# Kernel tuning notes

Measured on AMD Instinct MI355X. Metric: run time of the kernel, lower is better.

Reference implementation:

```python
import jax, jax.numpy as jnp
import numpy as np

EPS = 1e-5
D = 32          # token embedding dim
HEADS = 8
DH = D // HEADS  # 4


def _layernorm(x, g, b):
    mu = jnp.mean(x, axis=-1, keepdims=True)
    var = jnp.mean(jnp.square(x - mu), axis=-1, keepdims=True)
    return (x - mu) / jnp.sqrt(var + EPS) * g + b


def _mhsa(x, Wqvk, W0):
    # x: [..., t, 32]; Wqvk: [96, 32]; W0: [32, 32]
    qkv = x @ Wqvk.T                                   # [..., t, 96]
    qkv = qkv.reshape(qkv.shape[:-1] + (DH, 3, HEADS))  # (d k h) layout of original rearrange
    q, k, v = qkv[..., 0, :], qkv[..., 1, :], qkv[..., 2, :]  # [..., t, d, h]
    scores = jnp.einsum('...tdh,...sdh->...hts', q, k) * (DH ** -0.5)
    attn = jax.nn.softmax(scores, axis=-1)
    out = jnp.einsum('...hts,...sdh->...thd', attn, v)  # [..., t, h, d]
    out = out.reshape(out.shape[:-2] + (D,))            # (h d) concat order
    return out @ W0.T


def setup_inputs() -> dict:
    key = jax.random.key(0)
    ks = jax.random.split(key, 8)
    B = 256
    s = D ** -0.5
    return {
        'x':       jax.random.normal(ks[0], (B, 3, 32, 32, 32), dtype=jnp.float32),
        'pos_y':   jax.random.normal(ks[1], (3, 32, 32), dtype=jnp.float32) * s,
        'Wqvk_y':  jax.random.normal(ks[2], (3, 3 * D, D), dtype=jnp.float32) * s,
        'W0_y':    jax.random.normal(ks[3], (3, D, D), dtype=jnp.float32) * s,
        'g_y':     jnp.ones((D,), dtype=jnp.float32),
        'b_y':     jnp.zeros((D,), dtype=jnp.float32),
        'Wqvk_x':  jax.random.normal(ks[4], (3, 3 * D, D), dtype=jnp.float32) * s,
        'W0_x':    jax.random.normal(ks[5], (3, D, D), dtype=jnp.float32) * s,
        'g_x':     jnp.ones((D,), dtype=jnp.float32),
        'b_x':     jnp.zeros((D,), dtype=jnp.float32),
    }


def reference(x, pos_y, Wqvk_y, W0_y, g_y, b_y, Wqvk_x, W0_x, g_x, b_x):
    # x: [b, 3, l, w, h] with l=w=h=32. Dropout layers are in eval mode (identity).
    tst = jnp.transpose(x, (0, 1, 4, 2, 3))               # [b, 3, i(=h), t(=l), d(=w)]
    # AbsPosEmb1D per RGB channel: in_ @ pos^T
    emb = jnp.einsum('bcitd,cjd->bcitj', tst, pos_y)      # [b, 3, 32, 32, 32]
    outs = []
    for c in range(3):  # distinct r/g/b weights
        o = _mhsa(emb[:, c], Wqvk_y[c], W0_y[c])
        outs.append(_layernorm(emb[:, c] + o, g_y, b_y))
    x_tmp = jnp.stack(outs, axis=1)                       # [b, 3, i, t, 32]
    x_tmp = jnp.transpose(x_tmp, (0, 1, 3, 4, 2))         # [b, 3, t, 32, i]
    x1 = jax.nn.sigmoid(x_tmp) * x                        # first gating

    # BUG in original second loop: it reuses the stale `emb_y` from the last
    # iteration of the first loop (channel b, i = width-1) for every (i, j).
    emb_last = emb[:, 2, -1]                              # [b, 32, 32]
    ys = []
    for c in range(3):
        o = _mhsa(emb_last, Wqvk_x[c], W0_x[c])
        ys.append(_layernorm(emb_last + o, g_x, b_x))
    tmp2 = jnp.stack(ys, axis=1)                          # [b, 3, t, 32]
    # y stacked over i (constant across i), then permuted to [b,3,32,i,32]
    y_perm = jnp.transpose(tmp2, (0, 1, 3, 2))[:, :, :, None, :]  # [b,3,32,1,32]
    return jax.nn.sigmoid(y_perm) * x1
```

## Files before the change

kernel.cpp:

```cpp
#include <hip/hip_runtime.h>
#include <hip/hip_bf16.h>


using bf16 = __hip_bfloat16;
typedef float v2f __attribute__((ext_vector_type(2)));

__device__ __forceinline__ v2f pk_fma(v2f acc, v2f a, v2f b) {
  asm("v_pk_fma_f32 %0, %1, %2, %0" : "+v"(acc) : "v"(a), "v"(b));
  return acc;
}

template <int CTRL>
__device__ __forceinline__ float dpp_add(float x) {
  return x + __int_as_float(
      __builtin_amdgcn_mov_dpp(__float_as_int(x), CTRL, 0xF, 0xF, true));
}

struct __align__(16) SMem {
  float psJ[32][36];
  float wcF[96][36];
  float xs[32][32];
  float qS[32][36];
  float kT[32][36];
  float vT[32][36];
  float esT[32][34];
};

__global__ __launch_bounds__(256) void wc_kernel(
    const float* __restrict__ pos_y, const float* __restrict__ wqvk_y,
    const float* __restrict__ wqvk_x, float* __restrict__ wc)
{
  const int n = blockIdx.x;
  const int c = n % 3, xset = n / 3;
  const float* W = (xset ? wqvk_x : wqvk_y) + c * 3072;
  const float* P = pos_y + (xset ? 2 : c) * 1024;
  __shared__ float Ws[96][33];
  __shared__ float Ps[32][33];
  const int tid = threadIdx.x;
#pragma unroll
  for (int k = 0; k < 12; ++k) {
    const int e = tid * 12 + k;
    Ws[e >> 5][e & 31] = W[e];
  }
#pragma unroll
  for (int k = 0; k < 4; ++k) {
    const int e = tid * 4 + k;
    Ps[e >> 5][e & 31] = P[e];
  }
  __syncthreads();
  const int fg = tid >> 3, d0 = (tid & 7) * 4;
#pragma unroll
  for (int m = 0; m < 3; ++m) {
    const int f = fg + 32 * m;
    float s0 = 0.f, s1 = 0.f, s2 = 0.f, s3 = 0.f;
#pragma unroll
    for (int j = 0; j < 32; ++j) {
      const float w = Ws[f][j];
      s0 += w * Ps[j][d0];     s1 += w * Ps[j][d0 + 1];
      s2 += w * Ps[j][d0 + 2]; s3 += w * Ps[j][d0 + 3];
    }
    const float sc = ((f % 24) < 8) ? 0.72134752f : 1.0f;
    float* o = wc + (size_t)n * 3072 + f * 32 + d0;
    o[0] = s0 * sc; o[1] = s1 * sc; o[2] = s2 * sc; o[3] = s3 * sc;
  }
}

__device__ __forceinline__ void load_tables(
    SMem& sm, int tid, const float* __restrict__ xbc, int i,
    const float* __restrict__ pos, const float* __restrict__ wcg,
    const float* __restrict__ g, const float* __restrict__ b)
{
  const int t = tid >> 3, dq = (tid & 7) * 4;
  float xv0 = xbc[(t * 32 + dq + 0) * 32 + i];
  float xv1 = xbc[(t * 32 + dq + 1) * 32 + i];
  float xv2 = xbc[(t * 32 + dq + 2) * 32 + i];
  float xv3 = xbc[(t * 32 + dq + 3) * 32 + i];
  *(float4*)&sm.xs[t][dq] = make_float4(xv0, xv1, xv2, xv3);
  {
    const int e = tid * 4;
    float4 p = *(const float4*)&pos[e];
    *(float4*)&sm.psJ[e >> 5][e & 31] = p;
  }
  {
    float wf[12];
    *(float4*)&wf[0] = *(const float4*)&wcg[tid * 12];
    *(float4*)&wf[4] = *(const float4*)&wcg[tid * 12 + 4];
    *(float4*)&wf[8] = *(const float4*)&wcg[tid * 12 + 8];
#pragma unroll
    for (int k = 0; k < 6; ++k) {
      const int e = tid * 12 + 2 * k;
      *(v2f*)&sm.wcF[e >> 5][e & 31] = v2f{wf[2 * k], wf[2 * k + 1]};
    }
  }
  if (tid < 32) {
    sm.qS[tid][32] = g[tid] * 1.44269504f;
    sm.qS[tid][33] = b[tid] * 1.44269504f;
  }
}

__device__ __forceinline__ void mhsa_core(SMem& sm, int tid,
                                          const float* __restrict__ w0g,
                                          float sig_out[2][2])
{
  {
    const int u = tid >> 5, j = tid & 31;
    const int tR = 4 * u;
    float* sp[3]; int st[3];
#pragma unroll
    for (int m = 0; m < 3; ++m) {
      const int f = j + 32 * m;
      const int dh = f / 24, r2 = f - 24 * dh;
      const int sel = r2 >> 3, cc = (r2 & 7) * 4 + dh;
      if (sel == 0)      { sp[m] = &sm.qS[0][0] + cc;      st[m] = 36; }
      else if (sel == 1) { sp[m] = &sm.kT[0][0] + cc * 36; st[m] = 1;  }
      else               { sp[m] = &sm.vT[0][0] + cc * 36; st[m] = 1;  }
    }
    v2f ea[4], acc[3][4];
#pragma unroll
    for (int k = 0; k < 4; ++k) ea[k] = v2f{0.f, 0.f};
#pragma unroll
    for (int m = 0; m < 3; ++m)
#pragma unroll
      for (int k = 0; k < 4; ++k) acc[m][k] = v2f{0.f, 0.f};
#pragma unroll
    for (int d4 = 0; d4 < 8; ++d4) {
      float4 x0 = *(const float4*)&sm.xs[tR + 0][4 * d4];
      float4 x1 = *(const float4*)&sm.xs[tR + 1][4 * d4];
      float4 x2 = *(const float4*)&sm.xs[tR + 2][4 * d4];
      float4 x3 = *(const float4*)&sm.xs[tR + 3][4 * d4];
      float4 pj = *(const float4*)&sm.psJ[j][4 * d4];
      float4 wa = *(const float4*)&sm.wcF[j][4 * d4];
      float4 wb = *(const float4*)&sm.wcF[j + 32][4 * d4];
      float4 wc4 = *(const float4*)&sm.wcF[j + 64][4 * d4];
      v2f pl{pj.x, pj.y}, ph{pj.z, pj.w};
      v2f xl[4] = {v2f{x0.x,x0.y}, v2f{x1.x,x1.y}, v2f{x2.x,x2.y}, v2f{x3.x,x3.y}};
      v2f xh[4] = {v2f{x0.z,x0.w}, v2f{x1.z,x1.w}, v2f{x2.z,x2.w}, v2f{x3.z,x3.w}};
      v2f wl[3] = {v2f{wa.x,wa.y}, v2f{wb.x,wb.y}, v2f{wc4.x,wc4.y}};
      v2f wh[3] = {v2f{wa.z,wa.w}, v2f{wb.z,wb.w}, v2f{wc4.z,wc4.w}};
#pragma unroll
      for (int k = 0; k < 4; ++k) {
        ea[k] = pk_fma(ea[k], xl[k], pl);
        ea[k] = pk_fma(ea[k], xh[k], ph);
#pragma unroll
        for (int m = 0; m < 3; ++m) {
          acc[m][k] = pk_fma(acc[m][k], xl[k], wl[m]);
          acc[m][k] = pk_fma(acc[m][k], xh[k], wh[m]);
        }
      }
    }
    {
      const float e0 = ea[0][0] + ea[0][1], e1 = ea[1][0] + ea[1][1];
      const float e2 = ea[2][0] + ea[2][1], e3 = ea[3][0] + ea[3][1];
      *(v2f*)&sm.esT[j][tR]     = v2f{e0, e1};
      *(v2f*)&sm.esT[j][tR + 2] = v2f{e2, e3};
    }
#pragma unroll
    for (int m = 0; m < 3; ++m) {
      const float r0 = acc[m][0][0] + acc[m][0][1];
      const float r1 = acc[m][1][0] + acc[m][1][1];
      const float r2v = acc[m][2][0] + acc[m][2][1];
      const float r3 = acc[m][3][0] + acc[m][3][1];
      if (st[m] == 1) {
        *(float4*)(sp[m] + tR) = make_float4(r0, r1, r2v, r3);
      } else {
        sp[m][(tR + 0) * 36] = r0;
        sp[m][(tR + 1) * 36] = r1;
        sp[m][(tR + 2) * 36] = r2v;
        sp[m][(tR + 3) * 36] = r3;
      }
    }
  }
  float4 w0v = *(const float4*)&w0g[tid * 4];
  __syncthreads();
  {
    const int e = tid * 4;
    *(float4*)&sm.wcF[e >> 5][e & 31] = w0v;
  }

  {
    const int h = tid >> 5, tg2 = (tid >> 2) & 7, sg2 = tid & 3;
    const int ta = 4 * tg2, s0 = 8 * sg2;
    float4 qr0 = *(const float4*)&sm.qS[ta + 0][4 * h];
    float4 qr1 = *(const float4*)&sm.qS[ta + 1][4 * h];
    float4 qr2 = *(const float4*)&sm.qS[ta + 2][4 * h];
    float4 qr3 = *(const float4*)&sm.qS[ta + 3][4 * h];
    const float qa_[4][4] = {
        {qr0.x, qr0.y, qr0.z, qr0.w},
        {qr1.x, qr1.y, qr1.z, qr1.w},
        {qr2.x, qr2.y, qr2.z, qr2.w},
        {qr3.x, qr3.y, qr3.z, qr3.w}};
    v2f sc[4][4];
#pragma unroll
    for (int kk = 0; kk < 4; ++kk)
#pragma unroll
      for (int sp2 = 0; sp2 < 4; ++sp2) sc[kk][sp2] = v2f{0.f, 0.f};
#pragma unroll
    for (int dh = 0; dh < 4; ++dh) {
      const float* kr = &sm.kT[4 * h + dh][s0];
      float4 ka = *(const float4*)&kr[0];
      float4 kb = *(const float4*)&kr[4];
      v2f k0{ka.x, ka.y}, k1{ka.z, ka.w}, k2{kb.x, kb.y}, k3{kb.z, kb.w};
#pragma unroll
      for (int kk = 0; kk < 4; ++kk) {
        v2f qv{qa_[kk][dh], qa_[kk][dh]};
        sc[kk][0] = pk_fma(sc[kk][0], qv, k0);
        sc[kk][1] = pk_fma(sc[kk][1], qv, k1);
        sc[kk][2] = pk_fma(sc[kk][2], qv, k2);
        sc[kk][3] = pk_fma(sc[kk][3], qv, k3);
      }
    }
    float inv[4];
#pragma unroll
    for (int kk = 0; kk < 4; ++kk) {
#pragma unroll
      for (int sp2 = 0; sp2 < 4; ++sp2) {
        sc[kk][sp2][0] = exp2f(sc[kk][sp2][0]);
        sc[kk][sp2][1] = exp2f(sc[kk][sp2][1]);
      }
      v2f dv = sc[kk][0] + sc[kk][1];
      v2f dw = sc[kk][2] + sc[kk][3];
      dv += dw;
      float dn = dv[0] + dv[1];
      dn = dpp_add<0xB1>(dn);
      dn = dpp_add<0x4E>(dn);
      inv[kk] = __fdividef(1.0f, dn);
    }
    v2f pv[4][4];
#pragma unroll
    for (int kk = 0; kk < 4; ++kk)
#pragma unroll
      for (int dh = 0; dh < 4; ++dh) pv[kk][dh] = v2f{0.f, 0.f};
#pragma unroll
    for (int dh = 0; dh < 4; ++dh) {
      const float* vr = &sm.vT[4 * h + dh][s0];
      float4 va = *(const float4*)&vr[0];
      float4 vb = *(const float4*)&vr[4];
      v2f v0{va.x, va.y}, v1{va.z, va.w}, v2v{vb.x, vb.y}, v3{vb.z, vb.w};
#pragma unroll
      for (int kk = 0; kk < 4; ++kk) {
        pv[kk][dh] = pk_fma(pv[kk][dh], sc[kk][0], v0);
        pv[kk][dh] = pk_fma(pv[kk][dh], sc[kk][1], v1);
        pv[kk][dh] = pk_fma(pv[kk][dh], sc[kk][2], v2v);
        pv[kk][dh] = pk_fma(pv[kk][dh], sc[kk][3], v3);
      }
    }
    float ov[4][4];
#pragma unroll
    for (int kk = 0; kk < 4; ++kk)
#pragma unroll
      for (int dh = 0; dh < 4; ++dh) {
        float o = pv[kk][dh][0] + pv[kk][dh][1];
        o = dpp_add<0xB1>(o);
        o = dpp_add<0x4E>(o);
        ov[kk][dh] = o;
      }
    if (sg2 == 0) {
#pragma unroll
      for (int kk = 0; kk < 4; ++kk) {
        *(float4*)&sm.psJ[ta + kk][4 * h] = make_float4(
            ov[kk][0] * inv[kk], ov[kk][1] * inv[kk],
            ov[kk][2] * inv[kk], ov[kk][3] * inv[kk]);
      }
    }
  }
  __syncthreads();

  {
    const int g = tid >> 4, l = tid & 15;
    v2f a00{0.f,0.f}, a01{0.f,0.f}, a10{0.f,0.f}, a11{0.f,0.f};
#pragma unroll
    for (int f4 = 0; f4 < 8; ++f4) {
      float4 u0 = *(const float4*)&sm.psJ[g][4 * f4];
      float4 u1 = *(const float4*)&sm.psJ[g + 16][4 * f4];
      float4 w0 = *(const float4*)&sm.wcF[l][4 * f4];
      float4 w1 = *(const float4*)&sm.wcF[l + 16][4 * f4];
      a00 = pk_fma(a00, v2f{u0.x, u0.y}, v2f{w0.x, w0.y});
      a00 = pk_fma(a00, v2f{u0.z, u0.w}, v2f{w0.z, w0.w});
      a01 = pk_fma(a01, v2f{u0.x, u0.y}, v2f{w1.x, w1.y});
      a01 = pk_fma(a01, v2f{u0.z, u0.w}, v2f{w1.z, w1.w});
      a10 = pk_fma(a10, v2f{u1.x, u1.y}, v2f{w0.x, w0.y});
      a10 = pk_fma(a10, v2f{u1.z, u1.w}, v2f{w0.z, w0.w});
      a11 = pk_fma(a11, v2f{u1.x, u1.y}, v2f{w1.x, w1.y});
      a11 = pk_fma(a11, v2f{u1.z, u1.w}, v2f{w1.z, w1.w});
    }
    float rr[2][2];
    rr[0][0] = a00[0] + a00[1] + sm.esT[l][g];
    rr[0][1] = a01[0] + a01[1] + sm.esT[l + 16][g];
    rr[1][0] = a10[0] + a10[1] + sm.esT[l][g + 16];
    rr[1][1] = a11[0] + a11[1] + sm.esT[l + 16][g + 16];
    float s1a = rr[0][0] + rr[0][1], s1b = rr[1][0] + rr[1][1];
    float s2a = rr[0][0]*rr[0][0] + rr[0][1]*rr[0][1];
    float s2b = rr[1][0]*rr[1][0] + rr[1][1]*rr[1][1];
    s1a = dpp_add<0xB1>(s1a); s1a = dpp_add<0x4E>(s1a);
    s1a = dpp_add<0x124>(s1a); s1a = dpp_add<0x128>(s1a);
    s2a = dpp_add<0xB1>(s2a); s2a = dpp_add<0x4E>(s2a);
    s2a = dpp_add<0x124>(s2a); s2a = dpp_add<0x128>(s2a);
    s1b = dpp_add<0xB1>(s1b); s1b = dpp_add<0x4E>(s1b);
    s1b = dpp_add<0x124>(s1b); s1b = dpp_add<0x128>(s1b);
    s2b = dpp_add<0xB1>(s2b); s2b = dpp_add<0x4E>(s2b);
    s2b = dpp_add<0x124>(s2b); s2b = dpp_add<0x128>(s2b);
    const float mua = s1a * (1.0f / 32.0f), mub = s1b * (1.0f / 32.0f);
    const float ra = rsqrtf(s2a * (1.0f / 32.0f) - mua * mua + 1e-5f);
    const float rb = rsqrtf(s2b * (1.0f / 32.0f) - mub * mub + 1e-5f);
    const float g0 = sm.qS[l][32],      b0 = sm.qS[l][33];
    const float g1 = sm.qS[l + 16][32], b1 = sm.qS[l + 16][33];
    sig_out[0][0] = __fdividef(1.0f, 1.0f + exp2f(-((rr[0][0] - mua) * ra * g0 + b0)));
    sig_out[0][1] = __fdividef(1.0f, 1.0f + exp2f(-((rr[0][1] - mua) * ra * g1 + b1)));
    sig_out[1][0] = __fdividef(1.0f, 1.0f + exp2f(-((rr[1][0] - mub) * rb * g0 + b0)));
    sig_out[1][1] = __fdividef(1.0f, 1.0f + exp2f(-((rr[1][1] - mub) * rb * g1 + b1)));
  }
}

__global__ __launch_bounds__(256, 4) void phase1_kernel(
    const float* __restrict__ x, const float* __restrict__ pos_y,
    const float* __restrict__ wc, const float* __restrict__ w0_x,
    const float* __restrict__ g_x, const float* __restrict__ b_x,
    bf16* __restrict__ gates)
{
  __shared__ SMem sm;
  const int tid = threadIdx.x;
  const int n = blockIdx.x;
  const int c = n % 3, b = n / 3;
  const float* xbc = x + (size_t)(b * 3 + 2) * 32768;
  load_tables(sm, tid, xbc, 31, pos_y + 2 * 1024,
              wc + (size_t)(3 + c) * 3072, g_x, b_x);
  __syncthreads();
  float sig[2][2];
  mhsa_core(sm, tid, w0_x + c * 1024, sig);
  const int g = tid >> 4, l = tid & 15;
#pragma unroll
  for (int u = 0; u < 2; ++u)
#pragma unroll
    for (int v = 0; v < 2; ++v)
      gates[((c * 256 + b) * 32 + g + 16 * u) * 32 + l + 16 * v] =
          __float2bfloat16(sig[u][v]);
}

__global__ __launch_bounds__(256, 4) void phase2_kernel(
    const float* __restrict__ x, const float* __restrict__ pos_y,
    const float* __restrict__ wc, const float* __restrict__ w0_y,
    const float* __restrict__ g_y, const float* __restrict__ b_y,
    const bf16* __restrict__ gates, float* __restrict__ out)
{
  __shared__ SMem sm;
  const int tid = threadIdx.x;
  const int n = blockIdx.x;
  const int p = (n & 7) * 3072 + (n >> 3);
  const int i = p & 31, bc = p >> 5;
  const int c = bc % 3, b = bc / 3;
  const float* xbc = x + (size_t)bc * 32768;
  load_tables(sm, tid, xbc, i, pos_y + c * 1024,
              wc + (size_t)c * 3072, g_y, b_y);
  if (tid < 32)
    sm.kT[tid][32] = __bfloat162float(gates[((c * 256 + b) * 32 + i) * 32 + tid]);
  __syncthreads();
  float sig[2][2];
  mhsa_core(sm, tid, w0_y + c * 1024, sig);
  const int g = tid >> 4, l = tid & 15;
  float* ob = out + (size_t)bc * 32768 + i;
#pragma unroll
  for (int u = 0; u < 2; ++u) {
    const int r = g + 16 * u;
    const float sgv = sm.kT[r][32];
#pragma unroll
    for (int v = 0; v < 2; ++v) {
      const int cc = l + 16 * v;
      ob[(r * 32 + cc) * 32] = sgv * sig[u][v] * sm.xs[r][cc];
    }
  }
}

extern "C" void kernel_launch(void* const* d_in, const int* in_sizes, int n_in,
                              void* d_out, int out_size, void* d_ws, size_t ws_size,
                              hipStream_t stream) {
  const float* x      = (const float*)d_in[0];
  const float* pos_y  = (const float*)d_in[1];
  const float* wqvk_y = (const float*)d_in[2];
  const float* w0_y   = (const float*)d_in[3];
  const float* g_y    = (const float*)d_in[4];
  const float* b_y    = (const float*)d_in[5];
  const float* wqvk_x = (const float*)d_in[6];
  const float* w0_x   = (const float*)d_in[7];
  const float* g_x    = (const float*)d_in[8];
  const float* b_x    = (const float*)d_in[9];
  bf16*  gates = (bf16*)d_ws;
  float* wcbuf = (float*)((char*)d_ws + 1572864);

  hipLaunchKernelGGL(wc_kernel, dim3(6), dim3(256), 0, stream,
                     pos_y, wqvk_y, wqvk_x, wcbuf);
  hipLaunchKernelGGL(phase1_kernel, dim3(768), dim3(256), 0, stream,
                     x, pos_y, wcbuf, w0_x, g_x, b_x, gates);
  hipLaunchKernelGGL(phase2_kernel, dim3(24576), dim3(256), 0, stream,
                     x, pos_y, wcbuf, w0_y, g_y, b_y, gates, (float*)d_out);
}
```

Measured before the change: 446.1 us.

## Use split-bf16 MFMA for fused embedding and QKV projection

Replaces the FP32 packed-FMA projection of x onto pos and the combined QKV weights with bf16 MFMA 16x16x32 instructions. Precision is kept close to FP32 by a hi/lo split (three MFMAs per tile). The weight-prep kernel now emits split bf16 tables in an MFMA-friendly layout. Shared memory is reorganized with a union so the weight tiles and later attention buffers share space. This cuts VALU work in the dominant projection stage, at the cost of extra split conversions and some lost precision.

```diff
diff --git a/kernel.cpp b/kernel.cpp
--- a/kernel.cpp
+++ b/kernel.cpp
@@ -4,6 +4,8 @@
 
 using bf16 = __hip_bfloat16;
 typedef float v2f __attribute__((ext_vector_type(2)));
+using short8 = __attribute__((ext_vector_type(8))) short;
+using f32x4  = __attribute__((ext_vector_type(4))) float;
 
 __device__ __forceinline__ v2f pk_fma(v2f acc, v2f a, v2f b) {
   asm("v_pk_fma_f32 %0, %1, %2, %0" : "+v"(acc) : "v"(a), "v"(b));
@@ -16,22 +18,37 @@
       __builtin_amdgcn_mov_dpp(__float_as_int(x), CTRL, 0xF, 0xF, true));
 }
 
+__device__ __forceinline__ ushort bf16_rne(float f) {
+  uint u = __float_as_uint(f);
+  return (ushort)((u + 0x7FFFu + ((u >> 16) & 1u)) >> 16);
+}
+__device__ __forceinline__ void split2(float x, ushort& h, ushort& l) {
+  h = bf16_rne(x);
+  l = bf16_rne(x - __uint_as_float((uint)h << 16));
+}
+
 struct __align__(16) SMem {
-  float psJ[32][36];
-  float wcF[96][36];
-  float xs[32][32];
+  ushort xsH[32][40];
+  ushort xsL[32][40];
+  union {
+    struct { ushort WH[128][40]; ushort WL[128][40]; } w;
+    struct {
+      float esT[32][40];
+      float aoF[32][36];
+      float w0s[32][36];
+    } s;
+  } u;
   float qS[32][36];
   float kT[32][36];
   float vT[32][36];
-  float esT[32][34];
 };
 
 __global__ __launch_bounds__(256) void wc_kernel(
     const float* __restrict__ pos_y, const float* __restrict__ wqvk_y,
-    const float* __restrict__ wqvk_x, float* __restrict__ wc)
-{
-  const int n = blockIdx.x;
-  const int c = n % 3, xset = n / 3;
+    const float* __restrict__ wqvk_x, ushort* __restrict__ wc2)
+{
+  const int n6 = blockIdx.x;
+  const int c = n6 % 3, xset = n6 / 3;
   const float* W = (xset ? wqvk_x : wqvk_y) + c * 3072;
   const float* P = pos_y + (xset ? 2 : c) * 1024;
   __shared__ float Ws[96][33];
@@ -48,49 +65,56 @@
     Ps[e >> 5][e & 31] = P[e];
   }
   __syncthreads();
-  const int fg = tid >> 3, d0 = (tid & 7) * 4;
-#pragma unroll
-  for (int m = 0; m < 3; ++m) {
-    const int f = fg + 32 * m;
-    float s0 = 0.f, s1 = 0.f, s2 = 0.f, s3 = 0.f;
-#pragma unroll
-    for (int j = 0; j < 32; ++j) {
-      const float w = Ws[f][j];
-      s0 += w * Ps[j][d0];     s1 += w * Ps[j][d0 + 1];
-      s2 += w * Ps[j][d0 + 2]; s3 += w * Ps[j][d0 + 3];
-    }
-    const float sc = ((f % 24) < 8) ? 0.72134752f : 1.0f;
-    float* o = wc + (size_t)n * 3072 + f * 32 + d0;
-    o[0] = s0 * sc; o[1] = s1 * sc; o[2] = s2 * sc; o[3] = s3 * sc;
+  const int n = tid & 127, half = tid >> 7;
+  float src[16];
+  if (n >= 96) {
+    const int j = n - 96;
+#pragma unroll
+    for (int dd = 0; dd < 16; ++dd) src[dd] = Ps[j][16 * half + dd];
+  } else {
+    const int sidx = n >> 5;
+    const int m = n & 31, dh = m & 3, h = m >> 2;
+    const int f = dh * 24 + (sidx == 0 ? 8 : (sidx == 1 ? 16 : 0)) + h;
+    const float sc = (sidx == 2) ? 0.72134752f : 1.0f;
+#pragma unroll
+    for (int dd = 0; dd < 16; ++dd) {
+      float s = 0.f;
+      for (int j = 0; j < 32; ++j) s += Ws[f][j] * Ps[j][16 * half + dd];
+      src[dd] = s * sc;
+    }
+  }
+  ushort* base = wc2 + (size_t)n6 * 8192;
+#pragma unroll
+  for (int dd = 0; dd < 16; ++dd) {
+    ushort h, l;
+    split2(src[dd], h, l);
+    base[n * 32 + 16 * half + dd]        = h;
+    base[4096 + n * 32 + 16 * half + dd] = l;
   }
 }
 
 __device__ __forceinline__ void load_tables(
     SMem& sm, int tid, const float* __restrict__ xbc, int i,
-    const float* __restrict__ pos, const float* __restrict__ wcg,
+    const ushort* __restrict__ wc2,
     const float* __restrict__ g, const float* __restrict__ b)
 {
   const int t = tid >> 3, dq = (tid & 7) * 4;
-  float xv0 = xbc[(t * 32 + dq + 0) * 32 + i];
-  float xv1 = xbc[(t * 32 + dq + 1) * 32 + i];
-  float xv2 = xbc[(t * 32 + dq + 2) * 32 + i];
-  float xv3 = xbc[(t * 32 + dq + 3) * 32 + i];
-  *(float4*)&sm.xs[t][dq] = make_float4(xv0, xv1, xv2, xv3);
+  float xv[4];
+#pragma unroll
+  for (int k = 0; k < 4; ++k) xv[k] = xbc[(t * 32 + dq + k) * 32 + i];
+  ushort hs[4], ls[4];
+#pragma unroll
+  for (int k = 0; k < 4; ++k) split2(xv[k], hs[k], ls[k]);
+  *(short4*)&sm.xsH[t][dq] = make_short4((short)hs[0], (short)hs[1],
+                                         (short)hs[2], (short)hs[3]);
+  *(short4*)&sm.xsL[t][dq] = make_short4((short)ls[0], (short)ls[1],
+                                         (short)ls[2], (short)ls[3]);
   {
-    const int e = tid * 4;
-    float4 p = *(const float4*)&pos[e];
-    *(float4*)&sm.psJ[e >> 5][e & 31] = p;
-  }
-  {
-    float wf[12];
-    *(float4*)&wf[0] = *(const float4*)&wcg[tid * 12];
-    *(float4*)&wf[4] = *(const float4*)&wcg[tid * 12 + 4];
-    *(float4*)&wf[8] = *(const float4*)&wcg[tid * 12 + 8];
-#pragma unroll
-    for (int k = 0; k < 6; ++k) {
-      const int e = tid * 12 + 2 * k;
-      *(v2f*)&sm.wcF[e >> 5][e & 31] = v2f{wf[2 * k], wf[2 * k + 1]};
-    }
+    const float4* src = (const float4*)(wc2 + tid * 32);
+    float4 r0 = src[0], r1 = src[1], r2 = src[2], r3 = src[3];
+    ushort* dst = (tid < 128) ? &sm.u.w.WH[tid][0] : &sm.u.w.WL[tid - 128][0];
+    ((float4*)dst)[0] = r0; ((float4*)dst)[1] = r1;
+    ((float4*)dst)[2] = r2; ((float4*)dst)[3] = r3;
   }
   if (tid < 32) {
     sm.qS[tid][32] = g[tid] * 1.44269504f;
@@ -102,80 +126,49 @@
                                           const float* __restrict__ w0g,
                                           float sig_out[2][2])
 {
+  const int wv = tid >> 6, lane = tid & 63;
+  const int lr = lane & 15, lk = lane >> 4;
+  const int mt = wv >> 1;
+  const int qe = wv & 1;
+  const int t0 = mt * 16 + lk * 4;
+  f32x4 eC0 = {0.f,0.f,0.f,0.f}, eC1 = {0.f,0.f,0.f,0.f};
+
   {
-    const int u = tid >> 5, j = tid & 31;
-    const int tR = 4 * u;
-    float* sp[3]; int st[3];
-#pragma unroll
-    for (int m = 0; m < 3; ++m) {
-      const int f = j + 32 * m;
-      const int dh = f / 24, r2 = f - 24 * dh;
-      const int sel = r2 >> 3, cc = (r2 & 7) * 4 + dh;
-      if (sel == 0)      { sp[m] = &sm.qS[0][0] + cc;      st[m] = 36; }
-      else if (sel == 1) { sp[m] = &sm.kT[0][0] + cc * 36; st[m] = 1;  }
-      else               { sp[m] = &sm.vT[0][0] + cc * 36; st[m] = 1;  }
-    }
-    v2f ea[4], acc[3][4];
-#pragma unroll
-    for (int k = 0; k < 4; ++k) ea[k] = v2f{0.f, 0.f};
-#pragma unroll
-    for (int m = 0; m < 3; ++m)
-#pragma unroll
-      for (int k = 0; k < 4; ++k) acc[m][k] = v2f{0.f, 0.f};
-#pragma unroll
-    for (int d4 = 0; d4 < 8; ++d4) {
-      float4 x0 = *(const float4*)&sm.xs[tR + 0][4 * d4];
-      float4 x1 = *(const float4*)&sm.xs[tR + 1][4 * d4];
-      float4 x2 = *(const float4*)&sm.xs[tR + 2][4 * d4];
-      float4 x3 = *(const float4*)&sm.xs[tR + 3][4 * d4];
-      float4 pj = *(const float4*)&sm.psJ[j][4 * d4];
-      float4 wa = *(const float4*)&sm.wcF[j][4 * d4];
-      float4 wb = *(const float4*)&sm.wcF[j + 32][4 * d4];
-      float4 wc4 = *(const float4*)&sm.wcF[j + 64][4 * d4];
-      v2f pl{pj.x, pj.y}, ph{pj.z, pj.w};
-      v2f xl[4] = {v2f{x0.x,x0.y}, v2f{x1.x,x1.y}, v2f{x2.x,x2.y}, v2f{x3.x,x3.y}};
-      v2f xh[4] = {v2f{x0.z,x0.w}, v2f{x1.z,x1.w}, v2f{x2.z,x2.w}, v2f{x3.z,x3.w}};
-      v2f wl[3] = {v2f{wa.x,wa.y}, v2f{wb.x,wb.y}, v2f{wc4.x,wc4.y}};
-      v2f wh[3] = {v2f{wa.z,wa.w}, v2f{wb.z,wb.w}, v2f{wc4.z,wc4.w}};
-#pragma unroll
-      for (int k = 0; k < 4; ++k) {
-        ea[k] = pk_fma(ea[k], xl[k], pl);
-        ea[k] = pk_fma(ea[k], xh[k], ph);
-#pragma unroll
-        for (int m = 0; m < 3; ++m) {
-          acc[m][k] = pk_fma(acc[m][k], xl[k], wl[m]);
-          acc[m][k] = pk_fma(acc[m][k], xh[k], wh[m]);
-        }
-      }
-    }
-    {
-      const float e0 = ea[0][0] + ea[0][1], e1 = ea[1][0] + ea[1][1];
-      const float e2 = ea[2][0] + ea[2][1], e3 = ea[3][0] + ea[3][1];
-      *(v2f*)&sm.esT[j][tR]     = v2f{e0, e1};
-      *(v2f*)&sm.esT[j][tR + 2] = v2f{e2, e3};
-    }
-#pragma unroll
-    for (int m = 0; m < 3; ++m) {
-      const float r0 = acc[m][0][0] + acc[m][0][1];
-      const float r1 = acc[m][1][0] + acc[m][1][1];
-      const float r2v = acc[m][2][0] + acc[m][2][1];
-      const float r3 = acc[m][3][0] + acc[m][3][1];
-      if (st[m] == 1) {
-        *(float4*)(sp[m] + tR) = make_float4(r0, r1, r2v, r3);
-      } else {
-        sp[m][(tR + 0) * 36] = r0;
-        sp[m][(tR + 1) * 36] = r1;
-        sp[m][(tR + 2) * 36] = r2v;
-        sp[m][(tR + 3) * 36] = r3;
-      }
+    short8 aH = *(const short8*)&sm.xsH[mt * 16 + lr][lk * 8];
+    short8 aL = *(const short8*)&sm.xsL[mt * 16 + lr][lk * 8];
+    f32x4 acc[4];
+#pragma unroll
+    for (int q = 0; q < 4; ++q) {
+      const int n = qe * 64 + q * 16 + lr;
+      short8 bH = *(const short8*)&sm.u.w.WH[n][lk * 8];
+      short8 bL = *(const short8*)&sm.u.w.WL[n][lk * 8];
+      f32x4 c = {0.f, 0.f, 0.f, 0.f};
+      c = __builtin_amdgcn_mfma_f32_16x16x32_bf16(aH, bH, c, 0, 0, 0);
+      c = __builtin_amdgcn_mfma_f32_16x16x32_bf16(aH, bL, c, 0, 0, 0);
+      c = __builtin_amdgcn_mfma_f32_16x16x32_bf16(aL, bH, c, 0, 0, 0);
+      acc[q] = c;
+    }
+    if (qe == 0) {
+      *(f32x4*)&sm.kT[lr][t0]      = acc[0];
+      *(f32x4*)&sm.kT[lr + 16][t0] = acc[1];
+      *(f32x4*)&sm.vT[lr][t0]      = acc[2];
+      *(f32x4*)&sm.vT[lr + 16][t0] = acc[3];
+    } else {
+#pragma unroll
+      for (int r = 0; r < 4; ++r) {
+        sm.qS[t0 + r][lr]      = acc[0][r];
+        sm.qS[t0 + r][lr + 16] = acc[1][r];
+      }
+      eC0 = acc[2]; eC1 = acc[3];
     }
   }
   float4 w0v = *(const float4*)&w0g[tid * 4];
   __syncthreads();
-  {
-    const int e = tid * 4;
-    *(float4*)&sm.wcF[e >> 5][e & 31] = w0v;
-  }
+  if (qe == 1) {
+    *(f32x4*)&sm.u.s.esT[lr][t0]      = eC0;
+    *(f32x4*)&sm.u.s.esT[lr + 16][t0] = eC1;
+  }
+  { const int e = tid * 4; *(float4*)&sm.u.s.w0s[e >> 5][e & 31] = w0v; }
 
   {
     const int h = tid >> 5, tg2 = (tid >> 2) & 7, sg2 = tid & 3;
@@ -257,7 +250,7 @@
     if (sg2 == 0) {
 #pragma unroll
       for (int kk = 0; kk < 4; ++kk) {
-        *(float4*)&sm.psJ[ta + kk][4 * h] = make_float4(
+        *(float4*)&sm.u.s.aoF[ta + kk][4 * h] = make_float4(
             ov[kk][0] * inv[kk], ov[kk][1] * inv[kk],
             ov[kk][2] * inv[kk], ov[kk][3] * inv[kk]);
       }
@@ -270,10 +263,10 @@
     v2f a00{0.f,0.f}, a01{0.f,0.f}, a10{0.f,0.f}, a11{0.f,0.f};
 #pragma unroll
     for (int f4 = 0; f4 < 8; ++f4) {
-      float4 u0 = *(const float4*)&sm.psJ[g][4 * f4];
-      float4 u1 = *(const float4*)&sm.psJ[g + 16][4 * f4];
-      float4 w0 = *(const float4*)&sm.wcF[l][4 * f4];
-      float4 w1 = *(const float4*)&sm.wcF[l + 16][4 * f4];
+      float4 u0 = *(const float4*)&sm.u.s.aoF[g][4 * f4];
+      float4 u1 = *(const float4*)&sm.u.s.aoF[g + 16][4 * f4];
+      float4 w0 = *(const float4*)&sm.u.s.w0s[l][4 * f4];
+      float4 w1 = *(const float4*)&sm.u.s.w0s[l + 16][4 * f4];
       a00 = pk_fma(a00, v2f{u0.x, u0.y}, v2f{w0.x, w0.y});
       a00 = pk_fma(a00, v2f{u0.z, u0.w}, v2f{w0.z, w0.w});
       a01 = pk_fma(a01, v2f{u0.x, u0.y}, v2f{w1.x, w1.y});
@@ -284,10 +277,10 @@
       a11 = pk_fma(a11, v2f{u1.z, u1.w}, v2f{w1.z, w1.w});
     }
     float rr[2][2];
-    rr[0][0] = a00[0] + a00[1] + sm.esT[l][g];
-    rr[0][1] = a01[0] + a01[1] + sm.esT[l + 16][g];
-    rr[1][0] = a10[0] + a10[1] + sm.esT[l][g + 16];
-    rr[1][1] = a11[0] + a11[1] + sm.esT[l + 16][g + 16];
+    rr[0][0] = a00[0] + a00[1] + sm.u.s.esT[l][g];
+    rr[0][1] = a01[0] + a01[1] + sm.u.s.esT[l + 16][g];
+    rr[1][0] = a10[0] + a10[1] + sm.u.s.esT[l][g + 16];
+    rr[1][1] = a11[0] + a11[1] + sm.u.s.esT[l + 16][g + 16];
     float s1a = rr[0][0] + rr[0][1], s1b = rr[1][0] + rr[1][1];
     float s2a = rr[0][0]*rr[0][0] + rr[0][1]*rr[0][1];
     float s2b = rr[1][0]*rr[1][0] + rr[1][1]*rr[1][1];
@@ -312,8 +305,8 @@
 }
 
 __global__ __launch_bounds__(256, 4) void phase1_kernel(
-    const float* __restrict__ x, const float* __restrict__ pos_y,
-    const float* __restrict__ wc, const float* __restrict__ w0_x,
+    const float* __restrict__ x, const ushort* __restrict__ wc2,
+    const float* __restrict__ w0_x,
     const float* __restrict__ g_x, const float* __restrict__ b_x,
     bf16* __restrict__ gates)
 {
@@ -322,8 +315,7 @@
   const int n = blockIdx.x;
   const int c = n % 3, b = n / 3;
   const float* xbc = x + (size_t)(b * 3 + 2) * 32768;
-  load_tables(sm, tid, xbc, 31, pos_y + 2 * 1024,
-              wc + (size_t)(3 + c) * 3072, g_x, b_x);
+  load_tables(sm, tid, xbc, 31, wc2 + (size_t)(3 + c) * 8192, g_x, b_x);
   __syncthreads();
   float sig[2][2];
   mhsa_core(sm, tid, w0_x + c * 1024, sig);
@@ -337,8 +329,8 @@
 }
 
 __global__ __launch_bounds__(256, 4) void phase2_kernel(
-    const float* __restrict__ x, const float* __restrict__ pos_y,
-    const float* __restrict__ wc, const float* __restrict__ w0_y,
+    const float* __restrict__ x, const ushort* __restrict__ wc2,
+    const float* __restrict__ w0_y,
     const float* __restrict__ g_y, const float* __restrict__ b_y,
     const bf16* __restrict__ gates, float* __restrict__ out)
 {
@@ -349,8 +341,7 @@
   const int i = p & 31, bc = p >> 5;
   const int c = bc % 3, b = bc / 3;
   const float* xbc = x + (size_t)bc * 32768;
-  load_tables(sm, tid, xbc, i, pos_y + c * 1024,
-              wc + (size_t)c * 3072, g_y, b_y);
+  load_tables(sm, tid, xbc, i, wc2 + (size_t)c * 8192, g_y, b_y);
   if (tid < 32)
     sm.kT[tid][32] = __bfloat162float(gates[((c * 256 + b) * 32 + i) * 32 + tid]);
   __syncthreads();
@@ -365,7 +356,9 @@
 #pragma unroll
     for (int v = 0; v < 2; ++v) {
       const int cc = l + 16 * v;
-      ob[(r * 32 + cc) * 32] = sgv * sig[u][v] * sm.xs[r][cc];
+      const float xv = __uint_as_float((uint)sm.xsH[r][cc] << 16) +
+                       __uint_as_float((uint)sm.xsL[r][cc] << 16);
+      ob[(r * 32 + cc) * 32] = sgv * sig[u][v] * xv;
     }
   }
 }
@@ -383,13 +376,13 @@
   const float* w0_x   = (const float*)d_in[7];
   const float* g_x    = (const float*)d_in[8];
   const float* b_x    = (const float*)d_in[9];
-  bf16*  gates = (bf16*)d_ws;
-  float* wcbuf = (float*)((char*)d_ws + 1572864);
+  bf16*   gates = (bf16*)d_ws;
+  ushort* wc2   = (ushort*)((char*)d_ws + 1572864);
 
   hipLaunchKernelGGL(wc_kernel, dim3(6), dim3(256), 0, stream,
-                     pos_y, wqvk_y, wqvk_x, wcbuf);
+                     pos_y, wqvk_y, wqvk_x, wc2);
   hipLaunchKernelGGL(phase1_kernel, dim3(768), dim3(256), 0, stream,
-                     x, pos_y, wcbuf, w0_x, g_x, b_x, gates);
+                     x, wc2, w0_x, g_x, b_x, gates);
   hipLaunchKernelGGL(phase2_kernel, dim3(24576), dim3(256), 0, stream,
-                     x, pos_y, wcbuf, w0_y, g_y, b_y, gates, (float*)d_out);
-}
+                     x, wc2, w0_y, g_y, b_y, gates, (float*)d_out);
+}
```

Measured after the change: 400.8 us. 1.11x faster.
